# Performance work log

Measured on AMD Instinct MI355X. Metric: run time of the kernel, lower is better.

## Reference

```python
import jax, jax.numpy as jnp
import numpy as np

N_MELS = 80
SR = 24000
HOP = 256
NFFT = 1024
FBIN = NFFT // 2 + 1
B = 16
FRAMES = 800
T = FRAMES * HOP  # 204800 samples


def _mel_fb():
    # torchaudio-style HTK mel filterbank, (FBIN, N_MELS)
    all_freqs = np.linspace(0.0, SR / 2, FBIN)
    m_min = 2595.0 * np.log10(1.0)
    m_max = 2595.0 * np.log10(1.0 + (SR / 2) / 700.0)
    m_pts = np.linspace(m_min, m_max, N_MELS + 2)
    f_pts = 700.0 * (10.0 ** (m_pts / 2595.0) - 1.0)
    f_diff = f_pts[1:] - f_pts[:-1]
    slopes = f_pts[None, :] - all_freqs[:, None]
    down = -slopes[:, :-2] / f_diff[:-1]
    up = slopes[:, 2:] / f_diff[1:]
    return np.maximum(0.0, np.minimum(down, up))


def setup_inputs() -> dict:
    key = jax.random.key(0)
    k = jax.random.split(key, 6)
    f0 = 100.0 + 200.0 * jax.random.uniform(k[0], (B, FRAMES), dtype=jnp.float32)
    envelope_imp = jax.random.uniform(k[1], (B, N_MELS, FRAMES), dtype=jnp.float32)
    envelope_noi = jax.random.uniform(k[2], (B, N_MELS, FRAMES), dtype=jnp.float32)
    vocal_cord = jax.random.normal(k[3], (B, 256), dtype=jnp.float32) * 0.1
    reverb = jax.random.normal(k[4], (B, 8192), dtype=jnp.float32) * 0.02
    noise = jax.random.normal(k[5], (B, T), dtype=jnp.float32)
    n = jnp.arange(NFFT, dtype=jnp.float32)
    hann_window = 0.5 - 0.5 * jnp.cos(2.0 * jnp.pi * n / NFFT)  # periodic hann
    inv_mel = jnp.asarray(np.linalg.pinv(_mel_fb().T), dtype=jnp.float32)  # (FBIN, N_MELS)
    return {"f0": f0, "envelope_imp": envelope_imp, "envelope_noi": envelope_noi,
            "vocal_cord": vocal_cord, "reverb": reverb, "noise": noise,
            "hann_window": hann_window, "inv_mel": inv_mel}


def _upsample_linear(x, scale):
    # F.interpolate(mode='linear', align_corners=False): x (B,N) -> (B,N*scale)
    N = x.shape[1]
    pos = (jnp.arange(N * scale, dtype=jnp.float32) + 0.5) / scale - 0.5
    pos = jnp.clip(pos, 0.0, N - 1)
    i0 = jnp.floor(pos).astype(jnp.int32)
    i1 = jnp.minimum(i0 + 1, N - 1)
    w = pos - i0
    return x[:, i0] * (1.0 - w) + x[:, i1] * w


def _stft(x, window):
    # torch.stft(center=True, pad_mode='reflect', onesided) -> (B, FBIN, F)
    pad = NFFT // 2
    xp = jnp.pad(x, ((0, 0), (pad, pad)), mode='reflect')
    nframes = 1 + (xp.shape[1] - NFFT) // HOP
    idx = jnp.arange(nframes)[:, None] * HOP + jnp.arange(NFFT)[None, :]
    frames = xp[:, idx] * window  # (B, F, NFFT)
    return jnp.fft.rfft(frames, axis=-1).transpose(0, 2, 1)


def _istft(spec, window, length):
    # torch.istft overlap-add with window^2 envelope normalization
    frames = jnp.fft.irfft(spec.transpose(0, 2, 1), n=NFFT, axis=-1) * window  # (B,F,NFFT)
    nframes = frames.shape[1]
    L = HOP * (nframes - 1) + NFFT
    idx = (jnp.arange(nframes)[:, None] * HOP + jnp.arange(NFFT)[None, :]).reshape(-1)
    y = jnp.zeros((frames.shape[0], L), frames.dtype).at[:, idx].add(frames.reshape(frames.shape[0], -1))
    wsq = jnp.zeros((L,), window.dtype).at[idx].add(jnp.tile(window ** 2, nframes))
    pad = NFFT // 2
    y = y[:, pad:pad + length]
    wsq = wsq[pad:pad + length]
    return y / jnp.where(wsq > 1e-11, wsq, 1.0)


def _fft_convolve(signal, kernel):
    # DDSP-style centered FFT convolution; kernel zero-padded to signal length
    Tn = signal.shape[-1]
    k = jnp.pad(kernel, ((0, 0), (0, Tn - kernel.shape[-1])))
    s = jnp.pad(signal, ((0, 0), (0, Tn)))
    k = jnp.pad(k, ((0, 0), (Tn, 0)))
    out = jnp.fft.irfft(jnp.fft.rfft(s) * jnp.fft.rfft(k), n=2 * Tn)
    return out[..., Tn:]


def _minimum_phase(amp):
    # complex-cepstrum minimum-phase reconstruction along frequency axis (axis=1)
    log_amp = jnp.log(jnp.maximum(amp, 1e-6))
    cep = jnp.fft.irfft(log_amp, n=NFFT, axis=1)  # (B, NFFT, T)
    fold = jnp.concatenate([jnp.ones((1,)), 2.0 * jnp.ones((NFFT // 2 - 1,)),
                            jnp.ones((1,)), jnp.zeros((NFFT // 2 - 1,))]).astype(amp.dtype)
    return jnp.exp(jnp.fft.rfft(cep * fold[None, :, None], axis=1))


def reference(f0, envelope_imp, envelope_noi, vocal_cord, reverb, noise, hann_window, inv_mel):
    # --- no_grad excitation block ---
    f0 = jax.lax.stop_gradient(f0)
    noise = jax.lax.stop_gradient(noise)
    f0_up = _upsample_linear(f0, HOP)  # (B, T)
    imp_scale = jax.lax.rsqrt(jnp.maximum(f0_up, 20.0)) * np.float32(np.sqrt(SR))
    saw = jnp.mod(jnp.cumsum(f0_up, axis=1) / SR, 1.0)
    impulse = (saw - jnp.roll(saw, -1, axis=1) > 0.5).astype(f0.dtype)
    imp = impulse * imp_scale
    noi = noise * 0.33333
    # --- filtering ---
    imp = _fft_convolve(imp, vocal_cord)
    imp_stft = _stft(imp, hann_window)  # (B, FBIN, FRAMES+1) complex
    noi_stft = _stft(noi, hann_window)
    uv_mask = (jnp.pad(f0, ((0, 0), (1, 0)))[:, None, :] < 20.0).astype(jnp.float32)
    imp_stft = imp_stft + noi_stft * uv_mask
    kernel_imp = jax.nn.relu(jnp.einsum('fm,bmt->bft', inv_mel, envelope_imp))
    kernel_noi = jax.nn.relu(jnp.einsum('fm,bmt->bft', inv_mel, envelope_noi))
    kernel_imp = _minimum_phase(kernel_imp)
    kernel_imp = jnp.pad(kernel_imp, ((0, 0), (0, 0), (1, 0)))
    kernel_noi = jnp.pad(kernel_noi, ((0, 0), (0, 0), (1, 0)))
    voi_stft = imp_stft * kernel_imp + noi_stft * kernel_noi
    voi = _istft(voi_stft, hann_window, T)
    voi = _fft_convolve(voi, reverb)
    return voi
```

## Files before the change

kernel.cpp:

```cpp
#include <hip/hip_runtime.h>
#include <math.h>

#define B_   16
#define TT   204800
#define FRM  800
#define FB   513
#define FBP  516

__device__ __forceinline__ int PD2(int i) { return i + (i >> 4); }
__device__ __forceinline__ int r4(int g) {
  return ((g & 3) << 6) | ((g & 12) << 2) | ((g >> 2) & 12) | ((g >> 6) & 3);
}
__device__ __forceinline__ float2 cmul(float2 a, float2 b) {
  return make_float2(a.x * b.x - a.y * b.y, a.x * b.y + a.y * b.x);
}

__global__ void k_tw(float* tw) {
  int k = threadIdx.x;
  double a = -2.0 * 3.14159265358979323846 * (double)k / 1024.0;
  ((float2*)tw)[k] = make_float2((float)cos(a), (float)sin(a));
}

__global__ __launch_bounds__(256) void k_f0b(const float* __restrict__ f0, float* __restrict__ X,
                                             float* __restrict__ Pg) {
  int i = blockIdx.x * 256 + threadIdx.x;
  int b = i / 12800; int blk = i - b * 12800;
  int t0 = blk * 16;
  const float* fb = f0 + b * FRM;
  float xv[16];
  #pragma unroll
  for (int j = 0; j < 16; ++j) {
    int t = t0 + j;
    float p = __fsub_rn(__fadd_rn((float)t, 0.5f) / 256.0f, 0.5f);
    p = fminf(fmaxf(p, 0.0f), 799.0f);
    int i0 = (int)p;
    int i1 = i0 + 1; if (i1 > 799) i1 = 799;
    float w = __fsub_rn(p, (float)i0);
    float a = fb[i0], c = fb[i1];
    float p1 = a * (1.0f - w);
    float p2 = c * w;
    asm volatile("" : "+v"(p1), "+v"(p2));
    xv[j] = p1 + p2;
  }
  float* xo = X + (size_t)b * TT + t0;
  #pragma unroll
  for (int j = 0; j < 4; ++j)
    *(float4*)(xo + 4 * j) = make_float4(xv[4*j], xv[4*j+1], xv[4*j+2], xv[4*j+3]);
  float a = 0.0f;
  #pragma unroll
  for (int j = 0; j < 16; ++j) a = __fadd_rn(a, xv[j]);
  Pg[(size_t)b * TT + blk] = a;
}

__global__ __launch_bounds__(256) void k_scan_mid(float* __restrict__ Pg) {
  const int b = blockIdx.x;
  float* P = Pg + (size_t)b * TT;
  float* bsum0 = P;
  float* bsum1 = P + 25600;
  float* incl2 = P + 26400;
  float* bsum2 = P + 27200;
  float* incl3 = P + 27264;
  float* incl4 = P + 27328;
  const int tid = threadIdx.x;
  for (int i = tid; i < 800; i += 256) {
    float a = 0.0f;
    #pragma unroll
    for (int j = 0; j < 16; ++j) a = __fadd_rn(a, bsum0[i * 16 + j]);
    bsum1[i] = a;
  }
  __syncthreads();
  if (tid < 50) {
    float a = 0.0f;
    #pragma unroll
    for (int j = 0; j < 16; ++j) a = __fadd_rn(a, bsum1[tid * 16 + j]);
    bsum2[tid] = a;
  }
  __syncthreads();
  if (tid == 0) {
    float bs3[4];
    for (int i = 0; i < 4; ++i) {
      float a = 0.0f;
      for (int j = 0; j < 16; ++j) {
        int k = i * 16 + j;
        a = __fadd_rn(a, (k < 50) ? bsum2[k] : 0.0f);
      }
      bs3[i] = a;
    }
    float s = 0.0f;
    for (int i = 0; i < 4; ++i) { s = __fadd_rn(s, bs3[i]); incl4[i] = s; }
  }
  __syncthreads();
  if (tid < 50) {
    int blk = tid >> 4;
    float w = 0.0f;
    for (int j = blk * 16; j <= tid; ++j) w = __fadd_rn(w, bsum2[j]);
    float e = (blk == 0) ? 0.0f : incl4[blk - 1];
    incl3[tid] = __fadd_rn(e, w);
  }
  __syncthreads();
  for (int i = tid; i < 800; i += 256) {
    int blk = i >> 4;
    float w = 0.0f;
    for (int j = blk * 16; j <= i; ++j) w = __fadd_rn(w, bsum1[j]);
    float e = (blk == 0) ? 0.0f : incl3[blk - 1];
    incl2[i] = __fadd_rn(e, w);
  }
}

__global__ __launch_bounds__(256) void k_incl1(float* __restrict__ Pg) {
  int idx = blockIdx.x * 256 + threadIdx.x;
  int b = idx / 12800; int i = idx - b * 12800;
  float* P = Pg + (size_t)b * TT;
  const float* bsum0 = P;
  const float* incl2 = P + 26400;
  int blk = i >> 4;
  float w = 0.0f;
  for (int j = blk * 16; j <= i; ++j) w = __fadd_rn(w, bsum0[j]);
  float e = (blk == 0) ? 0.0f : incl2[blk - 1];
  P[12800 + i] = __fadd_rn(e, w);
}

__global__ __launch_bounds__(256) void k_scan_imp(const float* __restrict__ Xg, const float* __restrict__ Pg,
                                                  float* __restrict__ imp) {
  int idx = blockIdx.x * 256 + threadIdx.x;
  int b = idx / TT; int t = idx - b * TT;
  const float* x = Xg + (size_t)b * TT;
  const float* incl1 = Pg + (size_t)b * TT + 12800;
  int blk = t >> 4;
  float e = (blk == 0) ? 0.0f : incl1[blk - 1];
  float w = 0.0f;
  for (int j = blk * 16; j <= t; ++j) w = __fadd_rn(w, x[j]);
  float St = __fadd_rn(e, w);
  float st = St / 24000.0f;
  bool cross;
  if (t < TT - 1) {
    float St1 = ((t & 15) == 15) ? __fadd_rn(incl1[blk], x[t + 1])
                                 : __fadd_rn(e, __fadd_rn(w, x[t + 1]));
    cross = floorf(St1 / 24000.0f) > floorf(st);
  } else {
    float s0 = x[0] / 24000.0f;
    float sawt = __fsub_rn(st, floorf(st));
    float saw0 = __fsub_rn(s0, floorf(s0));
    cross = __fsub_rn(sawt, saw0) > 0.5f;
  }
  float v = 0.0f;
  if (cross) {
    float m = fmaxf(Xg[idx], 20.0f);
    v = 154.9193338f * (1.0f / sqrtf(m));
  }
  imp[idx] = v;
}

__global__ __launch_bounds__(256) void k_conv(const float* __restrict__ imp, const float* __restrict__ vc,
                                              float* __restrict__ outc) {
  int gid = blockIdx.x; int b = gid / 200; int tile = gid % 200; int t0 = tile * 1024;
  __shared__ float sx[1280 + 80];
  __shared__ float sv[256];
  int tid = threadIdx.x;
  sv[tid] = vc[b * 256 + tid];
  for (int idx = tid; idx < 1280; idx += 256) {
    int g = t0 - 256 + idx;
    sx[idx + (idx >> 4)] = (g >= 0) ? imp[(size_t)b * TT + g] : 0.0f;
  }
  __syncthreads();
  #define SXX(i) sx[(i) + ((i) >> 4)]
  int tl = tid * 4;
  int base = 256 + tl;
  float w0 = SXX(base), w1 = SXX(base + 1), w2 = SXX(base + 2), w3 = SXX(base + 3);
  float a0 = 0.0f, a1 = 0.0f, a2 = 0.0f, a3 = 0.0f;
  #pragma unroll 8
  for (int j = 0; j < 256; ++j) {
    float h = sv[j];
    a0 += h * w0; a1 += h * w1; a2 += h * w2; a3 += h * w3;
    w3 = w2; w2 = w1; w1 = w0;
    w0 = SXX(base - 1 - j);
  }
  *(float4*)(outc + (size_t)b * TT + t0 + tl) = make_float4(a0, a1, a2, a3);
  #undef SXX
}

__global__ __launch_bounds__(256) void k_dots(const float* __restrict__ invmel,
                                              const float* __restrict__ envi,
                                              const float* __restrict__ envn,
                                              float* __restrict__ la, float* __restrict__ kn) {
  const int NKT = 9, NFT = 13;
  int bid = blockIdx.x;
  int b = bid / (NKT * NFT);
  int r = bid % (NKT * NFT);
  int kt = r / NFT, ft = r % NFT;
  int k0 = kt * 64, f0 = ft * 64;
  __shared__ float at[80][68];
  int tid = threadIdx.x;
  {
    int kk = tid >> 2, mb = (tid & 3) * 20;
    int kg = k0 + kk;
    const float* src = invmel + kg * 80 + mb;
    #pragma unroll 5
    for (int q = 0; q < 20; ++q) at[mb + q][kk] = (kg < 513) ? src[q] : 0.0f;
  }
  __syncthreads();
  int tx = tid & 15, ty = tid >> 4;
  int fg0 = f0 + tx * 4;
  bool fok = fg0 < FRM;
  float ai[4][4], an[4][4];
  #pragma unroll
  for (int u = 0; u < 4; ++u)
    #pragma unroll
    for (int v = 0; v < 4; ++v) { ai[u][v] = 0.0f; an[u][v] = 0.0f; }
  if (fok) {
    const float* pi = envi + (size_t)b * 80 * FRM + fg0;
    const float* pn = envn + (size_t)b * 80 * FRM + fg0;
    #pragma unroll 4
    for (int m = 0; m < 80; ++m) {
      float4 a4 = *(const float4*)&at[m][ty * 4];
      float4 i4 = *(const float4*)(pi + (size_t)m * FRM);
      float4 n4 = *(const float4*)(pn + (size_t)m * FRM);
      float ar[4] = {a4.x, a4.y, a4.z, a4.w};
      float ir[4] = {i4.x, i4.y, i4.z, i4.w};
      float nr[4] = {n4.x, n4.y, n4.z, n4.w};
      #pragma unroll
      for (int u = 0; u < 4; ++u)
        #pragma unroll
        for (int v = 0; v < 4; ++v) { ai[u][v] += ar[u] * ir[v]; an[u][v] += ar[u] * nr[v]; }
    }
  }
  int kg = k0 + ty * 4;
  if (kg <= 512 && fok) {
    #pragma unroll
    for (int v = 0; v < 4; ++v) {
      int fg = fg0 + v;
      float4 vl, vk;
      vl.x = __logf(fmaxf(ai[0][v], 1e-6f)); vl.y = __logf(fmaxf(ai[1][v], 1e-6f));
      vl.z = __logf(fmaxf(ai[2][v], 1e-6f)); vl.w = __logf(fmaxf(ai[3][v], 1e-6f));
      vk.x = fmaxf(an[0][v], 0.0f); vk.y = fmaxf(an[1][v], 0.0f);
      vk.z = fmaxf(an[2][v], 0.0f); vk.w = fmaxf(an[3][v], 0.0f);
      *(float4*)(la + ((size_t)b * FRM + fg) * FBP + kg) = vl;
      *(float4*)(kn + ((size_t)b * FRM + fg) * FBP + kg) = vk;
    }
  }
}

__device__ __forceinline__ void fftc(float2* c, const float2* tw, bool inv) {
  int tid = threadIdx.x;
  __syncthreads();
  {
    int rb = r4(tid);
    float2 a0 = c[PD2(rb)], a1 = c[PD2(rb + 256)], a2 = c[PD2(rb + 512)], a3 = c[PD2(rb + 768)];
    __syncthreads();
    float t0r = a0.x + a2.x, t0i = a0.y + a2.y;
    float t1r = a0.x - a2.x, t1i = a0.y - a2.y;
    float t2r = a1.x + a3.x, t2i = a1.y + a3.y;
    float t3r = a1.x - a3.x, t3i = a1.y - a3.y;
    int base = tid << 2;
    c[PD2(base)]     = make_float2(t0r + t2r, t0i + t2i);
    c[PD2(base + 2)] = make_float2(t0r - t2r, t0i - t2i);
    if (!inv) {
      c[PD2(base + 1)] = make_float2(t1r + t3i, t1i - t3r);
      c[PD2(base + 3)] = make_float2(t1r - t3i, t1i + t3r);
    } else {
      c[PD2(base + 1)] = make_float2(t1r - t3i, t1i + t3r);
      c[PD2(base + 3)] = make_float2(t1r + t3i, t1i - t3r);
    }
    __syncthreads();
  }
  #pragma unroll
  for (int s = 1; s < 5; ++s) {
    int m = 1 << (2 * s);
    int pos = tid & (m - 1);
    int grp = tid >> (2 * s);
    int base = grp * (m << 2) + pos;
    int i0 = PD2(base), i1 = PD2(base + m), i2 = PD2(base + 2 * m), i3 = PD2(base + 3 * m);
    float2 a0 = c[i0], a1 = c[i1], a2 = c[i2], a3 = c[i3];
    {
      int r = 256 >> (2 * s);
      float2 w1 = tw[PD2(pos * r)];
      if (inv) w1.y = -w1.y;
      float2 w2 = cmul(w1, w1);
      float2 w3 = cmul(w2, w1);
      a1 = cmul(a1, w1); a2 = cmul(a2, w2); a3 = cmul(a3, w3);
    }
    float t0r = a0.x + a2.x, t0i = a0.y + a2.y;
    float t1r = a0.x - a2.x, t1i = a0.y - a2.y;
    float t2r = a1.x + a3.x, t2i = a1.y + a3.y;
    float t3r = a1.x - a3.x, t3i = a1.y - a3.y;
    c[i0] = make_float2(t0r + t2r, t0i + t2i);
    c[i2] = make_float2(t0r - t2r, t0i - t2i);
    if (!inv) {
      c[i1] = make_float2(t1r + t3i, t1i - t3r);
      c[i3] = make_float2(t1r - t3i, t1i + t3r);
    } else {
      c[i1] = make_float2(t1r - t3i, t1i + t3r);
      c[i3] = make_float2(t1r + t3i, t1i - t3r);
    }
    __syncthreads();
  }
}

#define LOAD_TWL() do { twl[PD2(tid)] = ((const float2*)twg)[tid]; } while (0)

__global__ __launch_bounds__(256) void k_minphase(const float* __restrict__ envimp, const float* __restrict__ invmel,
                                                  float* __restrict__ kimp, const float* __restrict__ twg,
                                                  const float* __restrict__ lab) {
  int gid = blockIdx.x; int b = gid / 400; int t0 = (gid % 400) * 2;
  __shared__ float2 c[1088], twl[272];
  __shared__ float envc[160];
  int tid = threadIdx.x;
  LOAD_TWL();
  if (!lab && tid < 160) {
    int mm = tid >> 1, fr2 = tid & 1;
    envc[tid] = envimp[((size_t)b * 80 + mm) * FRM + t0 + fr2];
  }
  __syncthreads();
  if (lab) {
    const float* l1 = lab + ((size_t)b * FRM + t0) * FBP;
    const float* l2 = lab + ((size_t)b * FRM + t0 + 1) * FBP;
    for (int f = tid; f < 513; f += 256) {
      float la1 = l1[f], la2 = l2[f];
      c[PD2(f)] = make_float2(la1, la2);
      if (f >= 1 && f <= 511) c[PD2(1024 - f)] = make_float2(la1, la2);
    }
  } else {
    for (int f = tid; f < 513; f += 256) {
      const float4* iv = (const float4*)(invmel + f * 80);
      float d1 = 0.0f, d2 = 0.0f;
      #pragma unroll 5
      for (int q = 0; q < 20; ++q) {
        float4 v = iv[q];
        d1 += v.x * envc[8*q]   + v.y * envc[8*q+2] + v.z * envc[8*q+4] + v.w * envc[8*q+6];
        d2 += v.x * envc[8*q+1] + v.y * envc[8*q+3] + v.z * envc[8*q+5] + v.w * envc[8*q+7];
      }
      float la1 = __logf(fmaxf(d1, 1e-6f));
      float la2 = __logf(fmaxf(d2, 1e-6f));
      c[PD2(f)] = make_float2(la1, la2);
      if (f >= 1 && f <= 511) c[PD2(1024 - f)] = make_float2(la1, la2);
    }
  }
  fftc(c, twl, true);
  for (int n = tid; n < 1024; n += 256) {
    float sn = ((n == 0 || n == 512) ? 1.0f : (n < 512 ? 2.0f : 0.0f)) * (1.0f / 1024.0f);
    int pn = PD2(n);
    c[pn].x *= sn; c[pn].y *= sn;
  }
  fftc(c, twl, false);
  for (int k = tid; k <= 512; k += 256) {
    int km = (1024 - k) & 1023;
    float2 z = c[PD2(k)], mm2 = c[PD2(km)];
    float f1r = 0.5f * (z.x + mm2.x), f1i = 0.5f * (z.y - mm2.y);
    float f2r = 0.5f * (z.y + mm2.y), f2i = 0.5f * (mm2.x - z.x);
    float e1 = __expf(f1r), e2 = __expf(f2r);
    float s1, c1, s2, c2;
    __sincosf(f1i, &s1, &c1);
    __sincosf(f2i, &s2, &c2);
    float2* o1 = (float2*)kimp + (size_t)(b * FRM + t0) * FB + k;
    float2* o2 = (float2*)kimp + (size_t)(b * FRM + t0 + 1) * FB + k;
    *o1 = make_float2(e1 * c1, e1 * s1);
    *o2 = make_float2(e2 * c2, e2 * s2);
  }
}

__global__ __launch_bounds__(256) void k_combine2(const float* __restrict__ impc, const float* __restrict__ noise,
                                                  const float* __restrict__ hann, const float* __restrict__ kimp,
                                                  const float* __restrict__ invmel, const float* __restrict__ envnoi,
                                                  float* __restrict__ frames, const float* __restrict__ twg,
                                                  const float* __restrict__ knb) {
  int gid = blockIdx.x; int b = gid / 400; int pr = gid % 400;
  int fA = 2 * pr + 1, fB = fA + 1;
  __shared__ float2 c[1088], twl[272], vvA[545], vvB[545];
  __shared__ float envA[80], envB[80];
  int tid = threadIdx.x;
  LOAD_TWL();
  if (!knb && tid < 160) {
    int mm = tid >> 1;
    if (tid & 1) envB[mm] = envnoi[((size_t)b * 80 + mm) * FRM + (fB - 1)];
    else         envA[mm] = envnoi[((size_t)b * 80 + mm) * FRM + (fA - 1)];
  }
  #pragma unroll
  for (int pass = 0; pass < 2; ++pass) {
    int f = pass ? fB : fA;
    for (int n = tid; n < 1024; n += 256) {
      int ip = f * 256 + n - 512;
      int ridx = ip < 0 ? -ip : (ip >= TT ? 2 * TT - 2 - ip : ip);
      float wv = hann[n];
      c[PD2(n)] = make_float2(impc[(size_t)b * TT + ridx] * wv,
                              noise[(size_t)b * TT + ridx] * 0.33333f * wv);
    }
    fftc(c, twl, false);
    const float* knrow = knb ? (knb + ((size_t)b * FRM + (f - 1)) * FBP) : nullptr;
    const float* env = pass ? envB : envA;
    float2* vv = pass ? vvB : vvA;
    for (int k = tid; k <= 512; k += 256) {
      int km = (1024 - k) & 1023;
      float2 z = c[PD2(k)], mm2 = c[PD2(km)];
      float Ir = 0.5f * (z.x + mm2.x), Ii = 0.5f * (z.y - mm2.y);
      float Nr = 0.5f * (z.y + mm2.y), Ni = 0.5f * (mm2.x - z.x);
      float2 kp = ((const float2*)kimp)[(size_t)(b * FRM + f - 1) * FB + k];
      float kn;
      if (knrow) {
        kn = knrow[k];
      } else {
        const float4* iv = (const float4*)(invmel + k * 80);
        float dot = 0.0f;
        #pragma unroll 5
        for (int q = 0; q < 20; ++q) {
          float4 v = iv[q];
          dot += v.x * env[4*q] + v.y * env[4*q+1] + v.z * env[4*q+2] + v.w * env[4*q+3];
        }
        kn = dot > 0.0f ? dot : 0.0f;
      }
      vv[PD2(k)] = make_float2(Ir * kp.x - Ii * kp.y + Nr * kn,
                               Ir * kp.y + Ii * kp.x + Ni * kn);
    }
    __syncthreads();
  }
  for (int n = tid; n < 1024; n += 256) {
    float2 v;
    if (n <= 512) {
      float2 a = vvA[PD2(n)], bb = vvB[PD2(n)];
      v = make_float2(a.x - bb.y, a.y + bb.x);
    } else {
      float2 a = vvA[PD2(1024 - n)], bb = vvB[PD2(1024 - n)];
      v = make_float2(a.x + bb.y, bb.x - a.y);
    }
    c[PD2(n)] = v;
  }
  fftc(c, twl, true);
  float* frA = frames + ((size_t)b * FRM + fA - 1) * 1024;
  float* frB = frames + ((size_t)b * FRM + fB - 1) * 1024;
  for (int n = tid; n < 1024; n += 256) {
    float2 y = c[PD2(n)];
    float hw = (1.0f / 1024.0f) * hann[n];
    frA[n] = y.x * hw;
    frB[n] = y.y * hw;
  }
}

__global__ __launch_bounds__(256) void k_ola(const float* __restrict__ frames, const float* __restrict__ hann,
                                             float* __restrict__ voi) {
  int idx = blockIdx.x * 256 + threadIdx.x;
  int b = idx / TT; int t2 = idx - b * TT;
  int i = t2 + 512;
  int fhi = i >> 8;
  float sum = 0.0f, wsq = 0.0f;
  for (int f = fhi - 3; f <= fhi; ++f) {
    if (f < 0 || f > 800) continue;
    int n = i - (f << 8);
    float wv = hann[n];
    wsq += wv * wv;
    if (f >= 1) sum += frames[((size_t)b * FRM + f - 1) * 1024 + n];
  }
  voi[idx] = sum / (wsq > 1e-11f ? wsq : 1.0f);
}

__global__ __launch_bounds__(256) void k_hspec(const float* __restrict__ rvb, float* __restrict__ hs,
                                               const float* __restrict__ twg) {
  int gid = blockIdx.x; int b = gid / 16; int p = gid % 16;
  __shared__ float2 c[1088], twl[272];
  int tid = threadIdx.x;
  LOAD_TWL();
  for (int n = tid; n < 1024; n += 256) {
    c[PD2(n)] = make_float2((n < 512) ? rvb[(size_t)b * 8192 + p * 512 + n] : 0.0f, 0.0f);
  }
  fftc(c, twl, false);
  for (int k = tid; k <= 512; k += 256) {
    ((float2*)hs)[(size_t)(b * 16 + p) * FB + k] = c[PD2(k)];
  }
}

__global__ __launch_bounds__(256) void k_xspec2(const float* __restrict__ voi, float* __restrict__ xs,
                                                const float* __restrict__ twg) {
  int gid = blockIdx.x; int b = gid / 200; int mA = 2 * (gid % 200);
  __shared__ float2 c[1088], twl[272];
  int tid = threadIdx.x;
  LOAD_TWL();
  const float* vb = voi + (size_t)b * TT;
  for (int n = tid; n < 1024; n += 256) {
    int gA = (mA - 1) * 512 + n;
    int gB = gA + 512;
    float xa = (gA >= 0) ? vb[gA] : 0.0f;
    float xb = vb[gB];
    c[PD2(n)] = make_float2(xa, xb);
  }
  fftc(c, twl, false);
  float2* xsA = (float2*)xs + (size_t)(b * 400 + mA) * FB;
  float2* xsB = (float2*)xs + (size_t)(b * 400 + mA + 1) * FB;
  for (int k = tid; k <= 512; k += 256) {
    int km = (1024 - k) & 1023;
    float2 z = c[PD2(k)], w = c[PD2(km)];
    xsA[k] = make_float2(0.5f * (z.x + w.x), 0.5f * (z.y - w.y));
    xsB[k] = make_float2(0.5f * (z.y + w.y), 0.5f * (w.x - z.x));
  }
}

__global__ __launch_bounds__(256) void k_r22(const float* __restrict__ xsp, const float* __restrict__ hsp,
                                             float* __restrict__ out, const float* __restrict__ twg) {
  int gid = blockIdx.x; int b = gid / 200; int mA = 2 * (gid % 200); int mB = mA + 1;
  __shared__ float2 c[1088], twl[272], vvA[545], vvB[545];
  int tid = threadIdx.x;
  LOAD_TWL();
  const float2* X = (const float2*)xsp + (size_t)b * 400 * FB;
  const float2* H = (const float2*)hsp + (size_t)b * 16 * FB;
  for (int k = tid; k <= 512; k += 256) {
    float arA = 0.0f, aiA = 0.0f, arB = 0.0f, aiB = 0.0f;
    #pragma unroll 4
    for (int jj = 0; jj <= 16; ++jj) {
      int j = mB - jj;
      if (j < 0) break;
      float2 xj = X[(size_t)j * FB + k];
      if (jj <= 15) {
        float2 h = H[(size_t)jj * FB + k];
        arB += xj.x * h.x - xj.y * h.y;
        aiB += xj.x * h.y + xj.y * h.x;
      }
      if (jj >= 1) {
        float2 h = H[(size_t)(jj - 1) * FB + k];
        arA += xj.x * h.x - xj.y * h.y;
        aiA += xj.x * h.y + xj.y * h.x;
      }
    }
    vvA[PD2(k)] = make_float2(arA, aiA);
    vvB[PD2(k)] = make_float2(arB, aiB);
  }
  __syncthreads();
  for (int n = tid; n < 1024; n += 256) {
    float2 v;
    if (n <= 512) {
      float2 a = vvA[PD2(n)], bb = vvB[PD2(n)];
      v = make_float2(a.x - bb.y, a.y + bb.x);
    } else {
      float2 a = vvA[PD2(1024 - n)], bb = vvB[PD2(1024 - n)];
      v = make_float2(a.x + bb.y, bb.x - a.y);
    }
    c[PD2(n)] = v;
  }
  fftc(c, twl, true);
  float* oA = out + (size_t)b * TT + mA * 512;
  float* oB = out + (size_t)b * TT + mB * 512;
  for (int n2 = tid; n2 < 512; n2 += 256) {
    float2 y = c[PD2(512 + n2)];
    oA[n2] = y.x * (1.0f / 1024.0f);
    oB[n2] = y.y * (1.0f / 1024.0f);
  }
}

extern "C" void kernel_launch(void* const* d_in, const int* in_sizes, int n_in,
                              void* d_out, int out_size, void* d_ws, size_t ws_size,
                              hipStream_t stream) {
  const float* f0   = (const float*)d_in[0];
  const float* envi = (const float*)d_in[1];
  const float* envn = (const float*)d_in[2];
  const float* vc   = (const float*)d_in[3];
  const float* rvb  = (const float*)d_in[4];
  const float* noi  = (const float*)d_in[5];
  const float* hann = (const float*)d_in[6];
  const float* iml  = (const float*)d_in[7];
  float* out = (float*)d_out;
  float* ws  = (float*)d_ws;

  size_t o = 0;
  float* bufX = ws + o; o += (size_t)B_ * TT;
  float* bufS = ws + o; o += (size_t)B_ * TT;
  float* bufK = ws + o; o += (size_t)B_ * FRM * FB * 2;
  float* bufF = ws + o; o += (size_t)B_ * FRM * 1024;
  float* bufT = ws + o; o += 600;
  float* bufKN = ws + o; o += (size_t)B_ * FRM * FBP;
  bool pre = (o * sizeof(float) <= ws_size);
  float* la = pre ? bufF : nullptr;
  float* kn = pre ? bufKN : nullptr;

  hipLaunchKernelGGL(k_tw,       dim3(1),     dim3(256),  0, stream, bufT);
  hipLaunchKernelGGL(k_f0b,      dim3(800),   dim3(256),  0, stream, f0, bufX, out);
  hipLaunchKernelGGL(k_scan_mid, dim3(16),    dim3(256),  0, stream, out);
  hipLaunchKernelGGL(k_incl1,    dim3(800),   dim3(256),  0, stream, out);
  hipLaunchKernelGGL(k_scan_imp, dim3(12800), dim3(256),  0, stream, bufX, out, bufS);
  hipLaunchKernelGGL(k_conv,     dim3(3200),  dim3(256),  0, stream, bufS, vc, bufX);
  if (pre)
    hipLaunchKernelGGL(k_dots,   dim3(16 * 9 * 13), dim3(256), 0, stream, iml, envi, envn, la, kn);
  hipLaunchKernelGGL(k_minphase, dim3(6400),  dim3(256),  0, stream, envi, iml, bufK, bufT, la);
  hipLaunchKernelGGL(k_combine2, dim3(6400),  dim3(256),  0, stream, bufX, noi, hann, bufK, iml, envn, bufF, bufT, kn);
  hipLaunchKernelGGL(k_ola,      dim3(12800), dim3(256),  0, stream, bufF, hann, bufS);
  hipLaunchKernelGGL(k_hspec,    dim3(256),   dim3(256),  0, stream, rvb, bufK, bufT);
  hipLaunchKernelGGL(k_xspec2,   dim3(3200),  dim3(256),  0, stream, bufS, bufF, bufT);
  hipLaunchKernelGGL(k_r22,      dim3(3200),  dim3(256),  0, stream, bufF, bufK, out, bufT);
}
```

Measured before the change: 365.9 us.

## Fuse minimum-phase kernel into STFT combine and stage envelopes in LDS for dots

Merges the minimum-phase cepstral kernel into the combine kernel, so each block computes its two frames' minimum-phase spectra in shared memory instead of writing and re-reading a large complex buffer in global memory. The k_dots GEMM now stages envelope tiles in LDS rather than reading float4 values straight from global memory per iteration. Buffer assignments are reshuffled, with la moved to bufK and the reverb spectrum placed after it. The fused kernel uses much more shared memory per block, which may lower occupancy.

```diff
diff --git a/kernel.cpp b/kernel.cpp
--- a/kernel.cpp
+++ b/kernel.cpp
@@ -189,7 +189,7 @@
   int r = bid % (NKT * NFT);
   int kt = r / NFT, ft = r % NFT;
   int k0 = kt * 64, f0 = ft * 64;
-  __shared__ float at[80][68];
+  __shared__ float at[80][68], bi[80][68], bn[80][68];
   int tid = threadIdx.x;
   {
     int kk = tid >> 2, mb = (tid & 3) * 20;
@@ -198,37 +198,48 @@
     #pragma unroll 5
     for (int q = 0; q < 20; ++q) at[mb + q][kk] = (kg < 513) ? src[q] : 0.0f;
   }
+  {
+    int m0 = tid >> 4;
+    int fc = (tid & 15) * 4;
+    for (int mm = m0; mm < 80; mm += 16) {
+      const float* pi = envi + ((size_t)b * 80 + mm) * FRM + f0 + fc;
+      const float* pn = envn + ((size_t)b * 80 + mm) * FRM + f0 + fc;
+      #pragma unroll
+      for (int q = 0; q < 4; ++q) {
+        int fg = f0 + fc + q;
+        float vi = 0.0f, vn = 0.0f;
+        if (fg < FRM) { vi = pi[q]; vn = pn[q]; }
+        bi[mm][fc + q] = vi;
+        bn[mm][fc + q] = vn;
+      }
+    }
+  }
   __syncthreads();
   int tx = tid & 15, ty = tid >> 4;
-  int fg0 = f0 + tx * 4;
-  bool fok = fg0 < FRM;
   float ai[4][4], an[4][4];
   #pragma unroll
   for (int u = 0; u < 4; ++u)
     #pragma unroll
     for (int v = 0; v < 4; ++v) { ai[u][v] = 0.0f; an[u][v] = 0.0f; }
-  if (fok) {
-    const float* pi = envi + (size_t)b * 80 * FRM + fg0;
-    const float* pn = envn + (size_t)b * 80 * FRM + fg0;
-    #pragma unroll 4
-    for (int m = 0; m < 80; ++m) {
-      float4 a4 = *(const float4*)&at[m][ty * 4];
-      float4 i4 = *(const float4*)(pi + (size_t)m * FRM);
-      float4 n4 = *(const float4*)(pn + (size_t)m * FRM);
-      float ar[4] = {a4.x, a4.y, a4.z, a4.w};
-      float ir[4] = {i4.x, i4.y, i4.z, i4.w};
-      float nr[4] = {n4.x, n4.y, n4.z, n4.w};
+  #pragma unroll 8
+  for (int m = 0; m < 80; ++m) {
+    float4 a4 = *(const float4*)&at[m][ty * 4];
+    float4 i4 = *(const float4*)&bi[m][tx * 4];
+    float4 n4 = *(const float4*)&bn[m][tx * 4];
+    float ar[4] = {a4.x, a4.y, a4.z, a4.w};
+    float ir[4] = {i4.x, i4.y, i4.z, i4.w};
+    float nr[4] = {n4.x, n4.y, n4.z, n4.w};
+    #pragma unroll
+    for (int u = 0; u < 4; ++u)
       #pragma unroll
-      for (int u = 0; u < 4; ++u)
-        #pragma unroll
-        for (int v = 0; v < 4; ++v) { ai[u][v] += ar[u] * ir[v]; an[u][v] += ar[u] * nr[v]; }
-    }
+      for (int v = 0; v < 4; ++v) { ai[u][v] += ar[u] * ir[v]; an[u][v] += ar[u] * nr[v]; }
   }
   int kg = k0 + ty * 4;
-  if (kg <= 512 && fok) {
+  if (kg <= 512) {
     #pragma unroll
     for (int v = 0; v < 4; ++v) {
-      int fg = fg0 + v;
+      int fg = f0 + tx * 4 + v;
+      if (fg >= FRM) continue;
       float4 vl, vk;
       vl.x = __logf(fmaxf(ai[0][v], 1e-6f)); vl.y = __logf(fmaxf(ai[1][v], 1e-6f));
       vl.z = __logf(fmaxf(ai[2][v], 1e-6f)); vl.w = __logf(fmaxf(ai[3][v], 1e-6f));
@@ -298,22 +309,31 @@
 
 #define LOAD_TWL() do { twl[PD2(tid)] = ((const float2*)twg)[tid]; } while (0)
 
-__global__ __launch_bounds__(256) void k_minphase(const float* __restrict__ envimp, const float* __restrict__ invmel,
-                                                  float* __restrict__ kimp, const float* __restrict__ twg,
-                                                  const float* __restrict__ lab) {
-  int gid = blockIdx.x; int b = gid / 400; int t0 = (gid % 400) * 2;
-  __shared__ float2 c[1088], twl[272];
-  __shared__ float envc[160];
+__global__ __launch_bounds__(256) void k_comb3(const float* __restrict__ impc, const float* __restrict__ noise,
+                                               const float* __restrict__ hann, const float* __restrict__ invmel,
+                                               const float* __restrict__ envimp, const float* __restrict__ envnoi,
+                                               float* __restrict__ frames, const float* __restrict__ twg,
+                                               const float* __restrict__ lab, const float* __restrict__ knb) {
+  int gid = blockIdx.x; int b = gid / 400; int pr = gid % 400;
+  int fA = 2 * pr + 1, fB = fA + 1;
+  int r0 = b * FRM + 2 * pr;
+  __shared__ float2 c[1088], twl[272], vvA[545], vvB[545], kpA[545], kpB[545];
+  __shared__ float envA[80], envB[80], envc[160];
   int tid = threadIdx.x;
   LOAD_TWL();
+  if (!knb && tid < 160) {
+    int mm = tid >> 1;
+    if (tid & 1) envB[mm] = envnoi[((size_t)b * 80 + mm) * FRM + (fB - 1)];
+    else         envA[mm] = envnoi[((size_t)b * 80 + mm) * FRM + (fA - 1)];
+  }
   if (!lab && tid < 160) {
     int mm = tid >> 1, fr2 = tid & 1;
-    envc[tid] = envimp[((size_t)b * 80 + mm) * FRM + t0 + fr2];
+    envc[tid] = envimp[((size_t)r0 / FRM * 0 + (size_t)b * 80 + mm) * FRM + 2 * pr + fr2];
   }
   __syncthreads();
   if (lab) {
-    const float* l1 = lab + ((size_t)b * FRM + t0) * FBP;
-    const float* l2 = lab + ((size_t)b * FRM + t0 + 1) * FBP;
+    const float* l1 = lab + (size_t)r0 * FBP;
+    const float* l2 = lab + (size_t)(r0 + 1) * FBP;
     for (int f = tid; f < 513; f += 256) {
       float la1 = l1[f], la2 = l2[f];
       c[PD2(f)] = make_float2(la1, la2);
@@ -351,29 +371,10 @@
     float s1, c1, s2, c2;
     __sincosf(f1i, &s1, &c1);
     __sincosf(f2i, &s2, &c2);
-    float2* o1 = (float2*)kimp + (size_t)(b * FRM + t0) * FB + k;
-    float2* o2 = (float2*)kimp + (size_t)(b * FRM + t0 + 1) * FB + k;
-    *o1 = make_float2(e1 * c1, e1 * s1);
-    *o2 = make_float2(e2 * c2, e2 * s2);
-  }
-}
-
-__global__ __launch_bounds__(256) void k_combine2(const float* __restrict__ impc, const float* __restrict__ noise,
-                                                  const float* __restrict__ hann, const float* __restrict__ kimp,
-                                                  const float* __restrict__ invmel, const float* __restrict__ envnoi,
-                                                  float* __restrict__ frames, const float* __restrict__ twg,
-                                                  const float* __restrict__ knb) {
-  int gid = blockIdx.x; int b = gid / 400; int pr = gid % 400;
-  int fA = 2 * pr + 1, fB = fA + 1;
-  __shared__ float2 c[1088], twl[272], vvA[545], vvB[545];
-  __shared__ float envA[80], envB[80];
-  int tid = threadIdx.x;
-  LOAD_TWL();
-  if (!knb && tid < 160) {
-    int mm = tid >> 1;
-    if (tid & 1) envB[mm] = envnoi[((size_t)b * 80 + mm) * FRM + (fB - 1)];
-    else         envA[mm] = envnoi[((size_t)b * 80 + mm) * FRM + (fA - 1)];
-  }
+    kpA[PD2(k)] = make_float2(e1 * c1, e1 * s1);
+    kpB[PD2(k)] = make_float2(e2 * c2, e2 * s2);
+  }
+  __syncthreads();
   #pragma unroll
   for (int pass = 0; pass < 2; ++pass) {
     int f = pass ? fB : fA;
@@ -388,12 +389,13 @@
     const float* knrow = knb ? (knb + ((size_t)b * FRM + (f - 1)) * FBP) : nullptr;
     const float* env = pass ? envB : envA;
     float2* vv = pass ? vvB : vvA;
+    const float2* kp_ = pass ? kpB : kpA;
     for (int k = tid; k <= 512; k += 256) {
       int km = (1024 - k) & 1023;
       float2 z = c[PD2(k)], mm2 = c[PD2(km)];
       float Ir = 0.5f * (z.x + mm2.x), Ii = 0.5f * (z.y - mm2.y);
       float Nr = 0.5f * (z.y + mm2.y), Ni = 0.5f * (mm2.x - z.x);
-      float2 kp = ((const float2*)kimp)[(size_t)(b * FRM + f - 1) * FB + k];
+      float2 kp = kp_[PD2(k)];
       float kn;
       if (knrow) {
         kn = knrow[k];
@@ -424,8 +426,8 @@
     c[PD2(n)] = v;
   }
   fftc(c, twl, true);
-  float* frA = frames + ((size_t)b * FRM + fA - 1) * 1024;
-  float* frB = frames + ((size_t)b * FRM + fB - 1) * 1024;
+  float* frA = frames + (size_t)r0 * 1024;
+  float* frB = frames + (size_t)(r0 + 1) * 1024;
   for (int n = tid; n < 1024; n += 256) {
     float2 y = c[PD2(n)];
     float hw = (1.0f / 1024.0f) * hann[n];
@@ -564,7 +566,8 @@
   float* bufT = ws + o; o += 600;
   float* bufKN = ws + o; o += (size_t)B_ * FRM * FBP;
   bool pre = (o * sizeof(float) <= ws_size);
-  float* la = pre ? bufF : nullptr;
+  float* la = pre ? bufK : nullptr;
+  float* hs = bufK + (size_t)B_ * FRM * FBP;
   float* kn = pre ? bufKN : nullptr;
 
   hipLaunchKernelGGL(k_tw,       dim3(1),     dim3(256),  0, stream, bufT);
@@ -575,10 +578,9 @@
   hipLaunchKernelGGL(k_conv,     dim3(3200),  dim3(256),  0, stream, bufS, vc, bufX);
   if (pre)
     hipLaunchKernelGGL(k_dots,   dim3(16 * 9 * 13), dim3(256), 0, stream, iml, envi, envn, la, kn);
-  hipLaunchKernelGGL(k_minphase, dim3(6400),  dim3(256),  0, stream, envi, iml, bufK, bufT, la);
-  hipLaunchKernelGGL(k_combine2, dim3(6400),  dim3(256),  0, stream, bufX, noi, hann, bufK, iml, envn, bufF, bufT, kn);
+  hipLaunchKernelGGL(k_comb3,    dim3(6400),  dim3(256),  0, stream, bufX, noi, hann, iml, envi, envn, bufF, bufT, la, kn);
   hipLaunchKernelGGL(k_ola,      dim3(12800), dim3(256),  0, stream, bufF, hann, bufS);
-  hipLaunchKernelGGL(k_hspec,    dim3(256),   dim3(256),  0, stream, rvb, bufK, bufT);
+  hipLaunchKernelGGL(k_hspec,    dim3(256),   dim3(256),  0, stream, rvb, hs, bufT);
   hipLaunchKernelGGL(k_xspec2,   dim3(3200),  dim3(256),  0, stream, bufS, bufF, bufT);
-  hipLaunchKernelGGL(k_r22,      dim3(3200),  dim3(256),  0, stream, bufF, bufK, out, bufT);
-}
+  hipLaunchKernelGGL(k_r22,      dim3(3200),  dim3(256),  0, stream, bufF, hs, out, bufT);
+}
```

Result: no change. 362.9 us (-0.8%).
